# Optimization experiments

Measured on AMD Instinct MI355X. Metric: run time of the kernel, lower is better.

## Reference

```python
import jax, jax.numpy as jnp
import numpy as np

B, S, D = 2, 2048, 2048
H = 16
KV_RANK, Q_RANK = 512, 1536
NOPE, ROPE_D, VD = 128, 64, 128
QK_D = NOPE + ROPE_D  # 192


def _rope(t, positions):
    # t: (B, H, S, d) with d even; rotate-half RoPE, theta=10000
    d = t.shape[-1]
    inv_freq = 1.0 / (10000.0 ** (jnp.arange(0, d, 2, dtype=jnp.float32) / d))
    ang = positions.astype(jnp.float32)[:, None] * inv_freq  # (S, d//2)
    cos, sin = jnp.cos(ang), jnp.sin(ang)                    # (S, d//2)
    t1, t2 = t[..., : d // 2], t[..., d // 2 :]
    return jnp.concatenate([t1 * cos - t2 * sin, t2 * cos + t1 * sin], axis=-1)


def setup_inputs() -> dict:
    key = jax.random.key(0)
    ks = jax.random.split(key, 10)
    sc = 0.02
    return {
        "x": jax.random.normal(ks[0], (B, S, D), dtype=jnp.float32),
        "positions": jnp.arange(S, dtype=jnp.int32),
        # torch.nn.Linear weights are (out_features, in_features)
        "Wq_down": jax.random.normal(ks[1], (Q_RANK, D), dtype=jnp.float32) * sc,
        "Wq_up": jax.random.normal(ks[2], (H * NOPE, Q_RANK), dtype=jnp.float32) * sc,
        "Wq_rope": jax.random.normal(ks[3], (H * ROPE_D, Q_RANK), dtype=jnp.float32) * sc,
        "Wkv_down": jax.random.normal(ks[4], (KV_RANK, D), dtype=jnp.float32) * sc,
        "Wk_up": jax.random.normal(ks[5], (H * NOPE, KV_RANK), dtype=jnp.float32) * sc,
        "Wv_up": jax.random.normal(ks[6], (H * VD, KV_RANK), dtype=jnp.float32) * sc,
        "Wk_rope": jax.random.normal(ks[7], (ROPE_D, D), dtype=jnp.float32) * sc,
        "Wo": jax.random.normal(ks[8], (D, H * VD), dtype=jnp.float32) * sc,
    }


def reference(x, positions, Wq_down, Wq_up, Wq_rope, Wkv_down, Wk_up, Wv_up, Wk_rope, Wo):
    bsz, seq_len, _ = x.shape

    # Query path: low-rank down, then nope + rope up-projections
    c_q = x @ Wq_down.T                                             # (B, S, Q_RANK)
    q_c = (c_q @ Wq_up.T).reshape(bsz, seq_len, H, NOPE).transpose(0, 2, 1, 3)
    q_r = (c_q @ Wq_rope.T).reshape(bsz, seq_len, H, ROPE_D).transpose(0, 2, 1, 3)
    q_r = _rope(q_r, positions)
    q = jnp.concatenate([q_c, q_r], axis=-1)                        # (B, H, S, QK_D)

    # KV path: shared latent, single rope head broadcast to all heads
    c_kv = x @ Wkv_down.T                                           # (B, S, KV_RANK)
    k_c = (c_kv @ Wk_up.T).reshape(bsz, seq_len, H, NOPE).transpose(0, 2, 1, 3)
    v_c = (c_kv @ Wv_up.T).reshape(bsz, seq_len, H, VD).transpose(0, 2, 1, 3)
    k_r = (x @ Wk_rope.T).reshape(bsz, seq_len, 1, ROPE_D).transpose(0, 2, 1, 3)
    k_r = _rope(k_r, positions)
    k_r = jnp.broadcast_to(k_r, (bsz, H, seq_len, ROPE_D))
    k = jnp.concatenate([k_c, k_r], axis=-1)                        # (B, H, S, QK_D)

    # Causal SDPA, scale = 1/sqrt(total qk head dim)
    scale = 1.0 / math.sqrt(QK_D) if False else QK_D ** -0.5
    scores = jnp.einsum("bhqd,bhkd->bhqk", q, k) * scale
    causal = jnp.tril(jnp.ones((seq_len, seq_len), dtype=bool))
    scores = jnp.where(causal, scores, jnp.finfo(scores.dtype).min)
    attn = jax.nn.softmax(scores, axis=-1)
    out = jnp.einsum("bhqk,bhkd->bhqd", attn, v_c)                  # (B, H, S, VD)

    out = out.transpose(0, 2, 1, 3).reshape(bsz, seq_len, H * VD)
    return out @ Wo.T                                               # (B, S, D)
```

## Files before the change

kernel.cpp:

```cpp
#include <hip/hip_runtime.h>
#include <cmath>

#define SLEN 2048

typedef __bf16 bf16x8 __attribute__((ext_vector_type(8)));
typedef float  f32x4  __attribute__((ext_vector_type(4)));

__device__ inline void gld16(const void* g, void* l) {
    __builtin_amdgcn_global_load_lds(
        (const __attribute__((address_space(1))) void*)(uintptr_t)g,
        (__attribute__((address_space(3))) void*)(unsigned)(uintptr_t)l, 16, 0, 0);
}

struct CvArgs {
    const float* src[9];
    __bf16*      dst[9];
    long         cum[10];
};
__global__ __launch_bounds__(256)
void convert_all(CvArgs a) {
    long i8 = ((long)blockIdx.x * 256 + threadIdx.x) * 8;
    if (i8 >= a.cum[9]) return;
    int s = 0;
#pragma unroll
    for (int k = 1; k < 9; k++) if (i8 >= a.cum[k]) s = k;
    long loc = i8 - a.cum[s];
    const float* sp = a.src[s] + loc;
    float4 u0 = *(const float4*)(sp);
    float4 u1 = *(const float4*)(sp + 4);
    bf16x8 o;
    o[0] = (__bf16)u0.x; o[1] = (__bf16)u0.y; o[2] = (__bf16)u0.z; o[3] = (__bf16)u0.w;
    o[4] = (__bf16)u1.x; o[5] = (__bf16)u1.y; o[6] = (__bf16)u1.z; o[7] = (__bf16)u1.w;
    *(bf16x8*)(a.dst[s] + loc) = o;
}

struct Outs { __bf16* a; __bf16* b; __bf16* c; float* f; };

__global__ __launch_bounds__(256, 2)
void gemm_nt(const __bf16* __restrict__ A, const __bf16* __restrict__ B,
             Outs o, const int* __restrict__ positions,
             int M, int N, int K, int mode, float scale) {
    __shared__ __bf16 As[128 * 64];
    __shared__ __bf16 Bs[128 * 64];
    int tid = threadIdx.x;
    int wave = tid >> 6, lane = tid & 63;
    int lane15 = lane & 15, quad = lane >> 4;
    int ri = lane >> 3, ci = lane & 7;
    int cg = ci ^ ri;
    int m0 = blockIdx.x * 128, n0 = blockIdx.y * 128;
    int wm = (wave & 1) * 64, wn = (wave >> 1) * 64;
    f32x4 acc[4][4] = {};

    for (int k0 = 0; k0 < K; k0 += 64) {
#pragma unroll
        for (int t = 0; t < 4; t++) {
            int rr = wave * 32 + t * 8;
            int r = rr + ri;
            gld16(A + (size_t)(m0 + r) * K + k0 + cg * 8, As + rr * 64);
            int br = n0 + r; if (br > N - 1) br = N - 1;
            gld16(B + (size_t)br * K + k0 + cg * 8, Bs + rr * 64);
        }
        __syncthreads();
#pragma unroll
        for (int kk = 0; kk < 64; kk += 32) {
            int jb = kk >> 3;
            bf16x8 af[4], bfr[4];
#pragma unroll
            for (int mt = 0; mt < 4; mt++) {
                int rA = wm + mt * 16 + lane15;
                af[mt] = *(bf16x8*)(As + rA * 64 + (((jb + quad) ^ (rA & 7)) << 3));
            }
#pragma unroll
            for (int nt = 0; nt < 4; nt++) {
                int rB = wn + nt * 16 + lane15;
                bfr[nt] = *(bf16x8*)(Bs + rB * 64 + (((jb + quad) ^ (rB & 7)) << 3));
            }
#pragma unroll
            for (int mt = 0; mt < 4; mt++)
#pragma unroll
                for (int nt = 0; nt < 4; nt++)
                    acc[mt][nt] = __builtin_amdgcn_mfma_f32_16x16x32_bf16(
                        af[mt], bfr[nt], acc[mt][nt], 0, 0, 0);
        }
        __syncthreads();
    }

    const float KLOG = 13.287712379549449f / 32.0f;

    if (mode == 8 && n0 == 2048) {
        if (wn == 0) {
#pragma unroll
            for (int mt = 0; mt < 4; mt++) {
                int row = m0 + wm + mt * 16 + quad * 4;
#pragma unroll
                for (int nt = 0; nt < 2; nt++) {
                    int i = nt * 16 + lane15;
                    float inv = exp2f(-(float)i * KLOG);
#pragma unroll
                    for (int r = 0; r < 4; r++) {
                        int tok = row + r;
                        float p = (float)positions[tok & (SLEN - 1)];
                        float sn, cs; sincosf(p * inv, &sn, &cs);
                        float t1 = acc[mt][nt][r], t2 = acc[mt][nt + 2][r];
                        float rot1 = t1 * cs - t2 * sn;
                        float rot2 = t2 * cs + t1 * sn;
                        size_t ob = (size_t)tok * 3072 + 128;
#pragma unroll
                        for (int hh = 0; hh < 16; hh++) {
                            o.c[ob + hh * 192 + i]      = (__bf16)rot1;
                            o.c[ob + hh * 192 + 32 + i] = (__bf16)rot2;
                        }
                    }
                }
            }
        }
        return;
    }
    if (mode == 9 && n0 >= 2048) {
        int hh = (n0 + wn - 2048) >> 6;
#pragma unroll
        for (int mt = 0; mt < 4; mt++) {
            int row = m0 + wm + mt * 16 + quad * 4;
#pragma unroll
            for (int nt = 0; nt < 2; nt++) {
                int i = nt * 16 + lane15;
                float inv = exp2f(-(float)i * KLOG);
#pragma unroll
                for (int r = 0; r < 4; r++) {
                    int tok = row + r;
                    float p = (float)positions[tok & (SLEN - 1)];
                    float sn, cs; sincosf(p * inv, &sn, &cs);
                    float t1 = acc[mt][nt][r], t2 = acc[mt][nt + 2][r];
                    size_t ob = (size_t)tok * 3072 + hh * 192 + 128;
                    o.a[ob + i]      = (__bf16)((t1 * cs - t2 * sn) * scale);
                    o.a[ob + 32 + i] = (__bf16)((t2 * cs + t1 * sn) * scale);
                }
            }
        }
        return;
    }

#pragma unroll
    for (int mt = 0; mt < 4; mt++) {
        int row = m0 + wm + mt * 16 + quad * 4;
#pragma unroll
        for (int nt = 0; nt < 4; nt++) {
            int col = n0 + wn + nt * 16 + lane15;
            if (col < N) {
#pragma unroll
                for (int r = 0; r < 4; r++) {
                    float v = acc[mt][nt][r];
                    size_t rw = (size_t)(row + r);
                    if (mode == 2) {
                        o.f[rw * N + col] = v;
                    } else if (mode == 8) {
                        if (col < 1536) o.a[rw * 1536 + col] = (__bf16)v;
                        else            o.b[rw * 512 + col - 1536] = (__bf16)v;
                    } else if (mode == 9) {
                        o.a[rw * 3072 + (col >> 7) * 192 + (col & 127)] =
                            (__bf16)(v * scale);
                    } else {
                        if (col < 2048)
                            o.a[rw * 3072 + (col >> 7) * 192 + (col & 127)] = (__bf16)v;
                        else {
                            int d = col - 2048;
                            o.b[((size_t)d * 2 + (rw >> 11)) * 2048 + (rw & 2047)] = (__bf16)v;
                        }
                    }
                }
            }
        }
    }
}

__global__ __launch_bounds__(256, 2)
void mla_attn(const __bf16* __restrict__ Q, const __bf16* __restrict__ K,
              const __bf16* __restrict__ Vt, __bf16* __restrict__ O) {
    __shared__ __bf16 Ks[64 * 192];
    __shared__ __bf16 Vs[128 * 64];
    __shared__ __bf16 Ps[4][32][72];
    int tid = threadIdx.x, wave = tid >> 6, lane = tid & 63;
    int lane15 = lane & 15, quad = lane >> 4;
    int h = blockIdx.y, b = blockIdx.z;
    int x = blockIdx.x;
    int qt = 15 - x;
    int q0 = qt * 128;
    const __bf16* Qb  = Q + (size_t)b * SLEN * 3072 + h * 192;
    const __bf16* Kb  = K + (size_t)b * SLEN * 3072 + h * 192;
    const __bf16* vtb = Vt + ((size_t)(h * 128) * 2 + b) * 2048;

    bf16x8 qf[2][6];
#pragma unroll
    for (int mt = 0; mt < 2; mt++) {
        int qrow = q0 + wave * 32 + mt * 16 + lane15;
#pragma unroll
        for (int kk = 0; kk < 6; kk++)
            qf[mt][kk] = *(const bf16x8*)(Qb + (size_t)qrow * 3072 + kk * 32 + quad * 8);
    }
    bf16x8 ones;
#pragma unroll
    for (int e = 0; e < 8; e++) ones[e] = (__bf16)1.0f;

    f32x4 o_acc[2][8] = {};
    float m_i[2][4], l_i[2][4];
#pragma unroll
    for (int mt = 0; mt < 2; mt++)
#pragma unroll
        for (int r = 0; r < 4; r++) { m_i[mt][r] = -3.0e38f; l_i[mt][r] = 0.0f; }

    for (int j0 = 0; j0 <= q0 + 64; j0 += 64) {
#pragma unroll
        for (int t = 0; t < 6; t++) {
            int sb = (wave * 6 + t) * 64;
            int slot = sb + lane;
            int r = slot / 24;
            int c = slot - r * 24;
            int cgk = (c & ~7) | ((c & 7) ^ (r & 7));
            gld16(Kb + (size_t)(j0 + r) * 3072 + cgk * 8, Ks + sb * 8);
        }
#pragma unroll
        for (int t = 0; t < 4; t++) {
            int sb = (wave * 4 + t) * 64;
            int slot = sb + lane;
            int r = slot >> 3, c = slot & 7;
            gld16(vtb + (size_t)r * 4096 + j0 + (c ^ (r & 7)) * 8, Vs + sb * 8);
        }
        __syncthreads();

        f32x4 acc[2][4] = {};
        __builtin_amdgcn_s_setprio(1);
#pragma unroll
        for (int kk = 0; kk < 6; kk++) {
#pragma unroll
            for (int nt = 0; nt < 4; nt++) {
                int n = nt * 16 + lane15;
                int j = kk * 4 + quad;
                int cl = (j & ~7) | ((j & 7) ^ (n & 7));
                bf16x8 kf = *(bf16x8*)(Ks + n * 192 + cl * 8);
#pragma unroll
                for (int mt = 0; mt < 2; mt++)
                    acc[mt][nt] = __builtin_amdgcn_mfma_f32_16x16x32_bf16(
                        qf[mt][kk], kf, acc[mt][nt], 0, 0, 0);
            }
        }
        __builtin_amdgcn_s_setprio(0);

        if (j0 >= q0) {
#pragma unroll
            for (int mt = 0; mt < 2; mt++) {
                int rowg = q0 + wave * 32 + mt * 16 + quad * 4;
#pragma unroll
                for (int nt = 0; nt < 4; nt++) {
                    int colg = j0 + nt * 16 + lane15;
#pragma unroll
                    for (int r = 0; r < 4; r++)
                        if (colg > rowg + r) acc[mt][nt][r] = -3.0e38f;
                }
            }
        }

        float mx[2][4];
        bool need = false;
#pragma unroll
        for (int mt = 0; mt < 2; mt++)
#pragma unroll
            for (int r = 0; r < 4; r++) {
                float v = fmaxf(fmaxf(acc[mt][0][r], acc[mt][1][r]),
                                fmaxf(acc[mt][2][r], acc[mt][3][r]));
                mx[mt][r] = v;
                need = need || (v > m_i[mt][r] + 24.0f);
            }
        if (__any(need)) {
#pragma unroll
            for (int mt = 0; mt < 2; mt++)
#pragma unroll
                for (int r = 0; r < 4; r++) {
                    float v = mx[mt][r];
#pragma unroll
                    for (int d = 8; d >= 1; d >>= 1) v = fmaxf(v, __shfl_xor(v, d));
                    float mn = fmaxf(m_i[mt][r], v);
                    float alpha = exp2f(m_i[mt][r] - mn);
                    m_i[mt][r] = mn;
                    l_i[mt][r] *= alpha;
#pragma unroll
                    for (int nt = 0; nt < 8; nt++) o_acc[mt][nt][r] *= alpha;
                }
        }

#pragma unroll
        for (int mt = 0; mt < 2; mt++)
#pragma unroll
            for (int r = 0; r < 4; r++)
#pragma unroll
                for (int nt = 0; nt < 4; nt++) {
                    float pp = exp2f(acc[mt][nt][r] - m_i[mt][r]);
                    Ps[wave][mt * 16 + quad * 4 + r][nt * 16 + lane15] = (__bf16)pp;
                }

        f32x4 rs[2] = {};
        __builtin_amdgcn_s_setprio(1);
#pragma unroll
        for (int ks = 0; ks < 2; ks++) {
            bf16x8 pf[2];
#pragma unroll
            for (int mt = 0; mt < 2; mt++)
                pf[mt] = *(bf16x8*)(&Ps[wave][mt * 16 + lane15][ks * 32 + quad * 8]);
#pragma unroll
            for (int nt = 0; nt < 8; nt++) {
                int nn = nt * 16 + lane15;
                int j = ks * 4 + quad;
                bf16x8 vf = *(bf16x8*)(Vs + nn * 64 + (j ^ (nn & 7)) * 8);
#pragma unroll
                for (int mt = 0; mt < 2; mt++)
                    o_acc[mt][nt] = __builtin_amdgcn_mfma_f32_16x16x32_bf16(
                        pf[mt], vf, o_acc[mt][nt], 0, 0, 0);
            }
#pragma unroll
            for (int mt = 0; mt < 2; mt++)
                rs[mt] = __builtin_amdgcn_mfma_f32_16x16x32_bf16(
                    pf[mt], ones, rs[mt], 0, 0, 0);
        }
        __builtin_amdgcn_s_setprio(0);
#pragma unroll
        for (int mt = 0; mt < 2; mt++)
#pragma unroll
            for (int r = 0; r < 4; r++) l_i[mt][r] += rs[mt][r];
        __syncthreads();
    }

    int tokb = b * SLEN + q0 + wave * 32 + quad * 4;
#pragma unroll
    for (int mt = 0; mt < 2; mt++) {
#pragma unroll
        for (int r = 0; r < 4; r++) {
            float inv_l = 1.0f / l_i[mt][r];
            int tok = tokb + mt * 16 + r;
#pragma unroll
            for (int nt = 0; nt < 8; nt++) {
                O[(size_t)tok * 2048 + h * 128 + nt * 16 + lane15] =
                    (__bf16)(o_acc[mt][nt][r] * inv_l);
            }
        }
    }
}

extern "C" void kernel_launch(void* const* d_in, const int* in_sizes, int n_in,
                              void* d_out, int out_size, void* d_ws, size_t ws_size,
                              hipStream_t stream) {
    (void)in_sizes; (void)n_in; (void)out_size; (void)ws_size;
    const int* pos = (const int*)d_in[1];
    float* out = (float*)d_out;

    char* ws = (char*)d_ws;
    size_t off = 0;
    auto alloc = [&](size_t bytes) {
        char* p = ws + off;
        off += (bytes + 255) & ~(size_t)255;
        return p;
    };
    __bf16* x_bf  = (__bf16*)alloc(8388608ull * 2);
    __bf16* Wcat1 = (__bf16*)alloc(4325376ull * 2);
    __bf16* Wcat2 = (__bf16*)alloc(4718592ull * 2);
    __bf16* Wcat3 = (__bf16*)alloc(4194304ull * 2);
    __bf16* Wob   = (__bf16*)alloc(4194304ull * 2);
    __bf16* c_q   = (__bf16*)alloc(4096ull * 1536 * 2);
    __bf16* c_kv  = (__bf16*)alloc(4096ull * 512 * 2);
    __bf16* v_t   = (__bf16*)alloc(4096ull * 2048 * 2);
    __bf16* q_all = (__bf16*)alloc(4096ull * 3072 * 2);
    __bf16* k_all = (__bf16*)alloc(4096ull * 3072 * 2);
    __bf16* attn_o = (__bf16*)c_q;

    const float scale_l2 = 1.4426950408889634f / sqrtf(192.0f);
    dim3 blk(256);

    CvArgs cv;
    cv.src[0] = (const float*)d_in[0]; cv.dst[0] = x_bf;
    cv.src[1] = (const float*)d_in[2]; cv.dst[1] = Wcat1;
    cv.src[2] = (const float*)d_in[5]; cv.dst[2] = Wcat1 + 3145728;
    cv.src[3] = (const float*)d_in[8]; cv.dst[3] = Wcat1 + 4194304;
    cv.src[4] = (const float*)d_in[3]; cv.dst[4] = Wcat2;
    cv.src[5] = (const float*)d_in[4]; cv.dst[5] = Wcat2 + 3145728;
    cv.src[6] = (const float*)d_in[6]; cv.dst[6] = Wcat3;
    cv.src[7] = (const float*)d_in[7]; cv.dst[7] = Wcat3 + 1048576;
    cv.src[8] = (const float*)d_in[9]; cv.dst[8] = Wob;
    long ns[9] = {8388608, 3145728, 1048576, 131072, 3145728, 1572864,
                  1048576, 1048576, 4194304};
    cv.cum[0] = 0;
    for (int i = 0; i < 9; i++) cv.cum[i + 1] = cv.cum[i] + ns[i];
    convert_all<<<dim3((unsigned)(cv.cum[9] / 2048)), blk, 0, stream>>>(cv);

    Outs o1 = { c_q, c_kv, k_all, nullptr };
    gemm_nt<<<dim3(32, 17), blk, 0, stream>>>(x_bf, Wcat1, o1, pos, 4096, 2112, 2048, 8, 1.0f);
    Outs o2 = { q_all, nullptr, nullptr, nullptr };
    gemm_nt<<<dim3(32, 24), blk, 0, stream>>>(c_q, Wcat2, o2, pos, 4096, 3072, 1536, 9, scale_l2);
    Outs o3 = { k_all, v_t, nullptr, nullptr };
    gemm_nt<<<dim3(32, 32), blk, 0, stream>>>(c_kv, Wcat3, o3, pos, 4096, 4096, 512, 10, 1.0f);
    mla_attn<<<dim3(16, 16, 2), blk, 0, stream>>>(q_all, k_all, v_t, attn_o);
    Outs o4 = { nullptr, nullptr, nullptr, out };
    gemm_nt<<<dim3(32, 16), blk, 0, stream>>>(attn_o, Wob, o4, pos, 4096, 2048, 2048, 2, 1.0f);
}
```

Measured before the change: 434.1 us.

## Add double-buffered 256x128 GEMM kernel with tile swizzle and rebalance attention ordering

Adds a new 512-thread GEMM kernel with 256x128 tiles, double-buffered LDS staging split into two half-steps so the next tile's global-to-LDS loads overlap MFMA work, MFMA priority raising, and an XCD-aware block index remap. The projection and output GEMMs now use this kernel, and the k-rope tail of the first GEMM is split into a separate launch of the old kernel through a new column offset. The attention kernel interleaves causal query tiles differently per batch to balance long and short tiles. The larger tiles raise LDS and register use and drop the column bounds check, which relies on N being a multiple of 128.

```diff
diff --git a/kernel.cpp b/kernel.cpp
--- a/kernel.cpp
+++ b/kernel.cpp
@@ -39,7 +39,7 @@
 __global__ __launch_bounds__(256, 2)
 void gemm_nt(const __bf16* __restrict__ A, const __bf16* __restrict__ B,
              Outs o, const int* __restrict__ positions,
-             int M, int N, int K, int mode, float scale) {
+             int M, int N, int K, int mode, float scale, int n_off) {
     __shared__ __bf16 As[128 * 64];
     __shared__ __bf16 Bs[128 * 64];
     int tid = threadIdx.x;
@@ -47,7 +47,7 @@
     int lane15 = lane & 15, quad = lane >> 4;
     int ri = lane >> 3, ci = lane & 7;
     int cg = ci ^ ri;
-    int m0 = blockIdx.x * 128, n0 = blockIdx.y * 128;
+    int m0 = blockIdx.x * 128, n0 = blockIdx.y * 128 + n_off;
     int wm = (wave & 1) * 64, wn = (wave >> 1) * 64;
     f32x4 acc[4][4] = {};
 
@@ -116,11 +116,111 @@
         }
         return;
     }
+}
+
+__global__ __launch_bounds__(512, 2)
+void gemm_nt2(const __bf16* __restrict__ A, const __bf16* __restrict__ B,
+              Outs o, const int* __restrict__ positions,
+              int N, int K, int mode, float scale) {
+    __shared__ __bf16 As[2][256 * 64];
+    __shared__ __bf16 Bs[2][128 * 64];
+    int tid = threadIdx.x;
+    int wave = tid >> 6, lane = tid & 63;
+    int lane15 = lane & 15, quad = lane >> 4;
+    int wr = wave >> 1, wc = wave & 1;
+    int lr = lane >> 3, lc = lane & 7;
+
+    int nblk = gridDim.x;
+    int qq = nblk >> 3;
+    int bid = blockIdx.x;
+    int wg = (bid & 7) * qq + (bid >> 3);
+    int m0 = (wg & 15) * 256;
+    int n0 = (wg >> 4) * 128;
+
+    f32x4 acc[4][4] = {};
+    int NT = K >> 6;
+
+    auto stageA = [&](int t, int k0, int buf) {
+        int rr = t * 64 + wave * 8;
+        int r = rr + lr;
+        int cg = lc ^ (r & 7);
+        gld16(A + (size_t)(m0 + r) * K + k0 + cg * 8, &As[buf][0] + rr * 64);
+    };
+    auto stageB = [&](int t, int k0, int buf) {
+        int rr = t * 64 + wave * 8;
+        int r = rr + lr;
+        int cg = lc ^ (r & 7);
+        int br = n0 + r; if (br > N - 1) br = N - 1;
+        gld16(B + (size_t)br * K + k0 + cg * 8, &Bs[buf][0] + rr * 64);
+    };
+
+#pragma unroll
+    for (int t = 0; t < 4; t++) stageA(t, 0, 0);
+#pragma unroll
+    for (int t = 0; t < 2; t++) stageB(t, 0, 0);
+    __syncthreads();
+
+    for (int t = 0; t < NT; t++) {
+        int cur = t & 1;
+        int k1 = (t + 1) << 6;
+        bool more = (t + 1) < NT;
+
+        if (more) { stageA(0, k1, cur ^ 1); stageA(1, k1, cur ^ 1); stageB(0, k1, cur ^ 1); }
+        {
+            bf16x8 af[4], bfr[4];
+#pragma unroll
+            for (int mt = 0; mt < 4; mt++) {
+                int rA = wr * 64 + mt * 16 + lane15;
+                af[mt] = *(bf16x8*)(&As[cur][0] + rA * 64 + ((quad ^ (rA & 7)) << 3));
+            }
+#pragma unroll
+            for (int nt = 0; nt < 4; nt++) {
+                int rB = wc * 64 + nt * 16 + lane15;
+                bfr[nt] = *(bf16x8*)(&Bs[cur][0] + rB * 64 + ((quad ^ (rB & 7)) << 3));
+            }
+            __builtin_amdgcn_s_setprio(1);
+#pragma unroll
+            for (int mt = 0; mt < 4; mt++)
+#pragma unroll
+                for (int nt = 0; nt < 4; nt++)
+                    acc[mt][nt] = __builtin_amdgcn_mfma_f32_16x16x32_bf16(
+                        af[mt], bfr[nt], acc[mt][nt], 0, 0, 0);
+            __builtin_amdgcn_s_setprio(0);
+        }
+        __builtin_amdgcn_s_barrier();
+
+        if (more) { stageA(2, k1, cur ^ 1); stageA(3, k1, cur ^ 1); stageB(1, k1, cur ^ 1); }
+        {
+            bf16x8 af[4], bfr[4];
+#pragma unroll
+            for (int mt = 0; mt < 4; mt++) {
+                int rA = wr * 64 + mt * 16 + lane15;
+                af[mt] = *(bf16x8*)(&As[cur][0] + rA * 64 + (((4 + quad) ^ (rA & 7)) << 3));
+            }
+#pragma unroll
+            for (int nt = 0; nt < 4; nt++) {
+                int rB = wc * 64 + nt * 16 + lane15;
+                bfr[nt] = *(bf16x8*)(&Bs[cur][0] + rB * 64 + (((4 + quad) ^ (rB & 7)) << 3));
+            }
+            __builtin_amdgcn_s_setprio(1);
+#pragma unroll
+            for (int mt = 0; mt < 4; mt++)
+#pragma unroll
+                for (int nt = 0; nt < 4; nt++)
+                    acc[mt][nt] = __builtin_amdgcn_mfma_f32_16x16x32_bf16(
+                        af[mt], bfr[nt], acc[mt][nt], 0, 0, 0);
+            __builtin_amdgcn_s_setprio(0);
+        }
+        __syncthreads();
+    }
+
+    const float KLOG = 13.287712379549449f / 32.0f;
+
     if (mode == 9 && n0 >= 2048) {
-        int hh = (n0 + wn - 2048) >> 6;
+        int hh = (n0 + wc * 64 - 2048) >> 6;
 #pragma unroll
         for (int mt = 0; mt < 4; mt++) {
-            int row = m0 + wm + mt * 16 + quad * 4;
+            int row = m0 + wr * 64 + mt * 16 + quad * 4;
 #pragma unroll
             for (int nt = 0; nt < 2; nt++) {
                 int i = nt * 16 + lane15;
@@ -142,30 +242,28 @@
 
 #pragma unroll
     for (int mt = 0; mt < 4; mt++) {
-        int row = m0 + wm + mt * 16 + quad * 4;
+        int row = m0 + wr * 64 + mt * 16 + quad * 4;
 #pragma unroll
         for (int nt = 0; nt < 4; nt++) {
-            int col = n0 + wn + nt * 16 + lane15;
-            if (col < N) {
-#pragma unroll
-                for (int r = 0; r < 4; r++) {
-                    float v = acc[mt][nt][r];
-                    size_t rw = (size_t)(row + r);
-                    if (mode == 2) {
-                        o.f[rw * N + col] = v;
-                    } else if (mode == 8) {
-                        if (col < 1536) o.a[rw * 1536 + col] = (__bf16)v;
-                        else            o.b[rw * 512 + col - 1536] = (__bf16)v;
-                    } else if (mode == 9) {
-                        o.a[rw * 3072 + (col >> 7) * 192 + (col & 127)] =
-                            (__bf16)(v * scale);
-                    } else {
-                        if (col < 2048)
-                            o.a[rw * 3072 + (col >> 7) * 192 + (col & 127)] = (__bf16)v;
-                        else {
-                            int d = col - 2048;
-                            o.b[((size_t)d * 2 + (rw >> 11)) * 2048 + (rw & 2047)] = (__bf16)v;
-                        }
+            int col = n0 + wc * 64 + nt * 16 + lane15;
+#pragma unroll
+            for (int r = 0; r < 4; r++) {
+                float v = acc[mt][nt][r];
+                size_t rw = (size_t)(row + r);
+                if (mode == 2) {
+                    o.f[rw * N + col] = v;
+                } else if (mode == 8) {
+                    if (col < 1536) o.a[rw * 1536 + col] = (__bf16)v;
+                    else            o.b[rw * 512 + col - 1536] = (__bf16)v;
+                } else if (mode == 9) {
+                    o.a[rw * 3072 + (col >> 7) * 192 + (col & 127)] =
+                        (__bf16)(v * scale);
+                } else {
+                    if (col < 2048)
+                        o.a[rw * 3072 + (col >> 7) * 192 + (col & 127)] = (__bf16)v;
+                    else {
+                        int d = col - 2048;
+                        o.b[((size_t)d * 2 + (rw >> 11)) * 2048 + (rw & 2047)] = (__bf16)v;
                     }
                 }
             }
@@ -183,7 +281,8 @@
     int lane15 = lane & 15, quad = lane >> 4;
     int h = blockIdx.y, b = blockIdx.z;
     int x = blockIdx.x;
-    int qt = 15 - x;
+    int qt0 = (x & 1) ? (x >> 1) : (15 - (x >> 1));
+    int qt = b ? (15 - qt0) : qt0;
     int q0 = qt * 128;
     const __bf16* Qb  = Q + (size_t)b * SLEN * 3072 + h * 192;
     const __bf16* Kb  = K + (size_t)b * SLEN * 3072 + h * 192;
@@ -372,6 +471,7 @@
 
     const float scale_l2 = 1.4426950408889634f / sqrtf(192.0f);
     dim3 blk(256);
+    dim3 blk2(512);
 
     CvArgs cv;
     cv.src[0] = (const float*)d_in[0]; cv.dst[0] = x_bf;
@@ -389,13 +489,15 @@
     for (int i = 0; i < 9; i++) cv.cum[i + 1] = cv.cum[i] + ns[i];
     convert_all<<<dim3((unsigned)(cv.cum[9] / 2048)), blk, 0, stream>>>(cv);
 
-    Outs o1 = { c_q, c_kv, k_all, nullptr };
-    gemm_nt<<<dim3(32, 17), blk, 0, stream>>>(x_bf, Wcat1, o1, pos, 4096, 2112, 2048, 8, 1.0f);
+    Outs o1 = { c_q, c_kv, nullptr, nullptr };
+    gemm_nt2<<<dim3(256), blk2, 0, stream>>>(x_bf, Wcat1, o1, pos, 2048, 2048, 8, 1.0f);
+    Outs o1b = { nullptr, nullptr, k_all, nullptr };
+    gemm_nt<<<dim3(32, 1), blk, 0, stream>>>(x_bf, Wcat1, o1b, pos, 4096, 2112, 2048, 8, 1.0f, 2048);
     Outs o2 = { q_all, nullptr, nullptr, nullptr };
-    gemm_nt<<<dim3(32, 24), blk, 0, stream>>>(c_q, Wcat2, o2, pos, 4096, 3072, 1536, 9, scale_l2);
+    gemm_nt2<<<dim3(384), blk2, 0, stream>>>(c_q, Wcat2, o2, pos, 3072, 1536, 9, scale_l2);
     Outs o3 = { k_all, v_t, nullptr, nullptr };
-    gemm_nt<<<dim3(32, 32), blk, 0, stream>>>(c_kv, Wcat3, o3, pos, 4096, 4096, 512, 10, 1.0f);
+    gemm_nt2<<<dim3(512), blk2, 0, stream>>>(c_kv, Wcat3, o3, pos, 4096, 512, 10, 1.0f);
     mla_attn<<<dim3(16, 16, 2), blk, 0, stream>>>(q_all, k_all, v_t, attn_o);
     Outs o4 = { nullptr, nullptr, nullptr, out };
-    gemm_nt<<<dim3(32, 16), blk, 0, stream>>>(attn_o, Wob, o4, pos, 4096, 2048, 2048, 2, 1.0f);
+    gemm_nt2<<<dim3(256), blk2, 0, stream>>>(attn_o, Wob, o4, pos, 2048, 2048, 2, 1.0f);
 }
```

Result: slower. 479.4 us (+10.4%).

## Double-buffer GEMM LDS loads, remap workgroups across XCDs, and interleave attention tile order

Applied to the files above, without the earlier changes.

The GEMM now keeps two LDS buffers and issues the next K-tile's global-to-LDS loads before computing the current one, waiting with explicit vmcnt counts, so load latency overlaps MFMA work. Workgroup IDs are permuted so that consecutive tiles land on the same XCD chunk, meant to improve L2 reuse. MFMA sections also get raised wave priority. The causal attention grid alternates long and short query tiles (mirrored per batch) to balance load across CUs. LDS use doubles, which may lower occupancy, and the hardcoded m0 mapping (wg&31) assumes M=4096 and a grid size divisible by 8.

```diff
diff --git a/kernel.cpp b/kernel.cpp
--- a/kernel.cpp
+++ b/kernel.cpp
@@ -40,27 +40,48 @@
 void gemm_nt(const __bf16* __restrict__ A, const __bf16* __restrict__ B,
              Outs o, const int* __restrict__ positions,
              int M, int N, int K, int mode, float scale) {
-    __shared__ __bf16 As[128 * 64];
-    __shared__ __bf16 Bs[128 * 64];
+    __shared__ __bf16 As[2][128 * 64];
+    __shared__ __bf16 Bs[2][128 * 64];
     int tid = threadIdx.x;
     int wave = tid >> 6, lane = tid & 63;
     int lane15 = lane & 15, quad = lane >> 4;
     int ri = lane >> 3, ci = lane & 7;
     int cg = ci ^ ri;
-    int m0 = blockIdx.x * 128, n0 = blockIdx.y * 128;
+
+    int nwg = gridDim.x * gridDim.y;
+    int lin = blockIdx.y * gridDim.x + blockIdx.x;
+    int chunk = nwg >> 3;
+    int wg = (lin & 7) * chunk + (lin >> 3);
+    int m0 = (wg & 31) * 128;
+    int n0 = (wg >> 5) * 128;
+
     int wm = (wave & 1) * 64, wn = (wave >> 1) * 64;
     f32x4 acc[4][4] = {};
 
-    for (int k0 = 0; k0 < K; k0 += 64) {
+    auto stage = [&](int k0, int buf) {
 #pragma unroll
         for (int t = 0; t < 4; t++) {
             int rr = wave * 32 + t * 8;
             int r = rr + ri;
-            gld16(A + (size_t)(m0 + r) * K + k0 + cg * 8, As + rr * 64);
+            gld16(A + (size_t)(m0 + r) * K + k0 + cg * 8, &As[buf][0] + rr * 64);
             int br = n0 + r; if (br > N - 1) br = N - 1;
-            gld16(B + (size_t)br * K + k0 + cg * 8, Bs + rr * 64);
-        }
-        __syncthreads();
+            gld16(B + (size_t)br * K + k0 + cg * 8, &Bs[buf][0] + rr * 64);
+        }
+    };
+
+    int NT = K >> 6;
+    stage(0, 0);
+    for (int t = 0; t < NT; t++) {
+        int cur = t & 1;
+        if (t + 1 < NT) {
+            stage((t + 1) << 6, cur ^ 1);
+            asm volatile("s_waitcnt vmcnt(8)" ::: "memory");
+        } else {
+            asm volatile("s_waitcnt vmcnt(0)" ::: "memory");
+        }
+        __builtin_amdgcn_sched_barrier(0);
+        __builtin_amdgcn_s_barrier();
+        __builtin_amdgcn_sched_barrier(0);
 #pragma unroll
         for (int kk = 0; kk < 64; kk += 32) {
             int jb = kk >> 3;
@@ -68,21 +89,24 @@
 #pragma unroll
             for (int mt = 0; mt < 4; mt++) {
                 int rA = wm + mt * 16 + lane15;
-                af[mt] = *(bf16x8*)(As + rA * 64 + (((jb + quad) ^ (rA & 7)) << 3));
+                af[mt] = *(bf16x8*)(&As[cur][0] + rA * 64 + (((jb + quad) ^ (rA & 7)) << 3));
             }
 #pragma unroll
             for (int nt = 0; nt < 4; nt++) {
                 int rB = wn + nt * 16 + lane15;
-                bfr[nt] = *(bf16x8*)(Bs + rB * 64 + (((jb + quad) ^ (rB & 7)) << 3));
-            }
+                bfr[nt] = *(bf16x8*)(&Bs[cur][0] + rB * 64 + (((jb + quad) ^ (rB & 7)) << 3));
+            }
+            __builtin_amdgcn_s_setprio(1);
 #pragma unroll
             for (int mt = 0; mt < 4; mt++)
 #pragma unroll
                 for (int nt = 0; nt < 4; nt++)
                     acc[mt][nt] = __builtin_amdgcn_mfma_f32_16x16x32_bf16(
                         af[mt], bfr[nt], acc[mt][nt], 0, 0, 0);
-        }
-        __syncthreads();
+            __builtin_amdgcn_s_setprio(0);
+        }
+        __builtin_amdgcn_sched_barrier(0);
+        __builtin_amdgcn_s_barrier();
     }
 
     const float KLOG = 13.287712379549449f / 32.0f;
@@ -183,7 +207,8 @@
     int lane15 = lane & 15, quad = lane >> 4;
     int h = blockIdx.y, b = blockIdx.z;
     int x = blockIdx.x;
-    int qt = 15 - x;
+    int qt0 = (x & 1) ? (x >> 1) : (15 - (x >> 1));
+    int qt = b ? (15 - qt0) : qt0;
     int q0 = qt * 128;
     const __bf16* Qb  = Q + (size_t)b * SLEN * 3072 + h * 192;
     const __bf16* Kb  = K + (size_t)b * SLEN * 3072 + h * 192;
```

After: 455.3 us. +4.9%, slower.
